# Performance work log

Measured on AMD Instinct MI355X. Metric: run time of the kernel, lower is better.

The kernel has to match this reference:

```python
import jax, jax.numpy as jnp
import numpy as np

PAD_ID, SOS_ID, EOS_ID = 0, 1, 2


def setup_inputs() -> dict:
    key = jax.random.key(0)
    ks = jax.random.split(key, 8)
    V, E, H, B = 16000, 256, 512, 8
    s = 0.05  # weight scale to keep softmax well-conditioned
    return {
        "hidden": jax.random.normal(ks[0], (1, B, H), dtype=jnp.float32),
        "embedding": jax.random.normal(ks[1], (V, E), dtype=jnp.float32) * s,
        "w_ih": jax.random.normal(ks[2], (3 * H, E), dtype=jnp.float32) * s,
        "w_hh": jax.random.normal(ks[3], (3 * H, H), dtype=jnp.float32) * s,
        "b_ih": jax.random.normal(ks[4], (3 * H,), dtype=jnp.float32) * s,
        "b_hh": jax.random.normal(ks[5], (3 * H,), dtype=jnp.float32) * s,
        "w_out": jax.random.normal(ks[6], (V, H), dtype=jnp.float32) * s,
        "b_out": jax.random.normal(ks[7], (V,), dtype=jnp.float32) * s,
        "lenseq": 12,
        "k": 5,
    }


def reference(hidden, embedding, w_ih, w_hh, b_ih, b_hh, w_out, b_out, lenseq, k):
    V, E = embedding.shape
    _, B, H = hidden.shape
    dt = hidden.dtype
    pad_onehot = jax.nn.one_hot(PAD_ID, V, dtype=dt)

    def gru_cell(x_emb, h):  # x_emb: (k,B,E), h: (k,B,H); torch nn.GRU gate order r,z,n
        gi = x_emb @ w_ih.T + b_ih
        gh = h @ w_hh.T + b_hh
        i_r, i_z, i_n = jnp.split(gi, 3, axis=-1)
        h_r, h_z, h_n = jnp.split(gh, 3, axis=-1)
        r = jax.nn.sigmoid(i_r + h_r)
        z = jax.nn.sigmoid(i_z + h_z)
        n = jnp.tanh(i_n + r * h_n)
        return (1.0 - z) * n + z * h

    def step(carry, i):
        x, h, prob, res, _ = carry
        done = (x == EOS_ID) | (x == PAD_ID)            # (k,B)
        emb = embedding[x]                               # (k,B,E)
        h_new = gru_cell(emb, h)                         # (k,B,H)
        probs = jax.nn.softmax(h_new @ w_out.T + b_out, axis=-1)  # (k,B,V)
        pred = jnp.where(done[..., None], pad_onehot, probs)
        h = jnp.where(done[..., None], h, h_new)
        res = res.at[:, i].set(pred)                     # store raw pred (pre prob-scaling), as torch.cat copies
        scores = pred * prob[..., None]                  # (k,B,V); prob stays all-ones, faithful to source
        flat = scores.transpose(1, 0, 2).reshape(B, k * V)  # beam-major flatten per batch elem
        _, idx = jax.lax.top_k(flat, k)                  # (B,k)
        beam = (idx // V).T                              # (k,B)
        tok = (idx % V).T                                # (k,B)
        res = jnp.take_along_axis(res, beam[:, None, :, None], axis=0)
        prob = jnp.take_along_axis(prob, beam, axis=0)
        h = jnp.take_along_axis(h, beam[..., None], axis=0)
        return (tok, h, prob, res, pred), None

    x0 = jnp.full((k, B), SOS_ID, dtype=jnp.int32)
    h0 = jnp.broadcast_to(hidden[0], (k, B, H))
    prob0 = jnp.ones((k, B), dtype=dt)
    res0 = jnp.zeros((k, lenseq, B, V), dtype=dt)
    pred0 = jnp.zeros((k, B, V), dtype=dt)

    (x, h, prob, res, pred), _ = jax.lax.scan(step, (x0, h0, prob0, res0, pred0), jnp.arange(lenseq))

    # final top-1 selection per batch element over (k*V) flat scores
    scores = pred * prob[..., None]
    flat = scores.transpose(1, 0, 2).reshape(B, k * V)
    best_beam = jnp.argmax(flat, axis=-1) // V           # (B,)
    out = jnp.take_along_axis(res, best_beam[None, None, :, None], axis=0)[0]  # (lenseq,B,V)
    return out
```

## Files before the change

### kernel.cpp

```cpp
#include <hip/hip_runtime.h>

#define V 16000
#define E 256
#define H 512
#define HP 516
#define BB 8
#define T 12
#define NB 250
#define NBS 256
#define TPB 1024
#define CPB 64
#define AGENT __HIP_MEMORY_SCOPE_AGENT

typedef float vfloat4 __attribute__((ext_vector_type(4)));


constexpr int W_FL   = CPB * 512;
constexpr int SH_OFF = W_FL;
constexpr int SP_OFF = SH_OFF + BB * HP;
constexpr int RS_OFF = SP_OFF + 64 * 48;
constexpr int RV_OFF = RS_OFF + 128;
constexpr int RI_OFF = RV_OFF + 128;
constexpr int SS_OFF = RI_OFF + 128;
constexpr int XN_OFF = SS_OFF + 8;
constexpr int X_OFF  = XN_OFF + 8;
constexpr int SMEM_FL = X_OFF + 8;
constexpr size_t SMEM_BYTES = (size_t)SMEM_FL * 4;

__device__ __forceinline__ float dot4(float4 a, float4 b) {
    return a.x * b.x + a.y * b.y + a.z * b.z + a.w * b.w;
}

__global__ __launch_bounds__(256) void kinit(const float* __restrict__ hidden,
                                             float* __restrict__ hA,
                                             int* __restrict__ cnt,
                                             int* __restrict__ epoch) {
    int idx = blockIdx.x * 256 + threadIdx.x;
    if (idx < BB * H) hA[idx] = hidden[idx];
    if (idx < 64 * 16) cnt[idx] = 0;
    if (idx == 0) epoch[0] = 0;
}

__device__ __forceinline__ void barA(int* __restrict__ cnt, int ep) {
    __syncthreads();
    if (blockIdx.x < 64 && threadIdx.x == 0)
        __hip_atomic_fetch_add(&cnt[(8 + (blockIdx.x & 1)) * 16], 1,
                               __ATOMIC_RELEASE, AGENT);
    if (threadIdx.x < 2) {
        while (__hip_atomic_load(&cnt[(8 + threadIdx.x) * 16],
                                 __ATOMIC_RELAXED, AGENT) < 32 * ep)
            __builtin_amdgcn_s_sleep(2);
    }
    __builtin_amdgcn_fence(__ATOMIC_ACQUIRE, "workgroup");
    __syncthreads();
}

__device__ __forceinline__ void barB(int* __restrict__ cnt, int ep) {
    __syncthreads();
    if (threadIdx.x == 0)
        __hip_atomic_fetch_add(&cnt[(blockIdx.x & 7) * 16], 1,
                               __ATOMIC_RELEASE, AGENT);
    if (threadIdx.x < 8) {
        int q = (threadIdx.x < 2) ? 32 : 31;
        while (__hip_atomic_load(&cnt[threadIdx.x * 16],
                                 __ATOMIC_RELAXED, AGENT) < q * ep)
            __builtin_amdgcn_s_sleep(2);
    }
    __builtin_amdgcn_fence(__ATOMIC_ACQUIRE, "workgroup");
    __syncthreads();
}

__global__ __launch_bounds__(TPB, 4) void kmain(
    const float* __restrict__ emb_tab,
    const float* __restrict__ w_ih,
    const float* __restrict__ w_hh,
    const float* __restrict__ b_ih,
    const float* __restrict__ b_hh,
    const float* __restrict__ w_out,
    const float* __restrict__ b_out,
    float* __restrict__ hA,
    float* __restrict__ hB,
    float* __restrict__ psum,
    float* __restrict__ pval,
    int* __restrict__ pidx,
    int* __restrict__ cnt,
    int* __restrict__ epoch,
    float* __restrict__ out)
{
    extern __shared__ float smem[];
    float* w_lds  = smem;
    float* s_h    = smem + SH_OFF;
    float* s_part = smem + SP_OFF;
    float* s_e    = smem + SP_OFF;
    float* s_rsum = smem + RS_OFF;
    float* s_rval = smem + RV_OFF;
    int*   s_ridx = (int*)(smem + RI_OFF);
    float* s_S    = smem + SS_OFF;
    int*   s_Xn   = (int*)(smem + XN_OFF);
    int*   s_X    = (int*)(smem + X_OFF);

    const int blk = blockIdx.x, tid = threadIdx.x;
    (void)epoch;

    for (int i = tid; i < CPB * 128; i += TPB) {
        int col = i >> 7;
        int q4  = (i & 127) << 2;
        int vv  = blk * CPB + col;
        float4 w4 = *(const float4*)(w_out + (size_t)vv * H + q4);
        int sw = q4 ^ ((col & 7) << 2) ^ (((q4 >> 5) & 7) << 2);
        *(float4*)(w_lds + col * 512 + sw) = w4;
    }
    if (tid < BB) s_X[tid] = 1;
    __syncthreads();

    const int lane = tid & 63;
    const int wv   = tid >> 6;
    const int rh   = lane & 3;
    const int kq   = (lane >> 2) & 15;
    const int rowhalf = wv & 1;
    const int cs   = wv >> 1;
    const int r    = rowhalf * 4 + rh;
    const int xw   = (cs ^ (kq & 7)) << 2;
    const int hswz = (kq & 7) << 2;

    float bo[8];
#pragma unroll
    for (int p = 0; p < 8; p++) bo[p] = b_out[blk * CPB + p * 8 + cs];

    for (int t = 0; t < T; t++) {
        const float* h_cur = (t & 1) ? hB : hA;
        float*       h_nxt = (t & 1) ? hA : hB;
        const int par = t & 1;

        if (blk < 64) {
            int hr = tid >> 7, k4 = (tid & 127) << 2;
            const unsigned long long* p =
                (const unsigned long long*)(h_cur + hr * H + k4);
            union { unsigned long long u; float f[2]; } c0, c1;
            c0.u = __hip_atomic_load(p,     __ATOMIC_RELAXED, AGENT);
            c1.u = __hip_atomic_load(p + 1, __ATOMIC_RELAXED, AGENT);
            *(float4*)(s_h + hr * HP + k4) =
                make_float4(c0.f[0], c0.f[1], c1.f[0], c1.f[1]);
        }
        __syncthreads();
        if (blk < 64 && tid < 512) {
            const int jl = tid >> 6;
            const int ar = (tid >> 3) & 7;
            const int kq8 = tid & 7;
            const int j  = blk * 8 + jl;
            const int pair = jl * 8 + ar;
            float gir = 0.f, giz = 0.f, gin = 0.f, ghr = 0.f, ghz = 0.f, ghn = 0.f;
            {
                const float* erow = emb_tab + (size_t)s_X[ar] * E;
                const float* w0 = w_ih + (size_t)j * E;
                const float* w1 = w0 + (size_t)H * E;
                const float* w2 = w1 + (size_t)H * E;
                const int k0 = kq8 * (E / 8);
                for (int k = 0; k < E / 8; k += 4) {
                    float4 ev = *(const float4*)(erow + k0 + k);
                    gir += dot4(*(const float4*)(w0 + k0 + k), ev);
                    giz += dot4(*(const float4*)(w1 + k0 + k), ev);
                    gin += dot4(*(const float4*)(w2 + k0 + k), ev);
                }
            }
            {
                const float* hrow = s_h + ar * HP;
                const float* w0 = w_hh + (size_t)j * H;
                const float* w1 = w0 + (size_t)H * H;
                const float* w2 = w1 + (size_t)H * H;
                const int k0 = kq8 * (H / 8);
                for (int k = 0; k < H / 8; k += 4) {
                    float4 hv = *(const float4*)(hrow + k0 + k);
                    ghr += dot4(*(const float4*)(w0 + k0 + k), hv);
                    ghz += dot4(*(const float4*)(w1 + k0 + k), hv);
                    ghn += dot4(*(const float4*)(w2 + k0 + k), hv);
                }
            }
            float* sp = s_part + pair * 48;
            sp[0 * 8 + kq8] = gir; sp[1 * 8 + kq8] = giz; sp[2 * 8 + kq8] = gin;
            sp[3 * 8 + kq8] = ghr; sp[4 * 8 + kq8] = ghz; sp[5 * 8 + kq8] = ghn;
        }
        __syncthreads();
        if (blk < 64 && tid < 512 && (tid & 7) == 0) {
            const int pair = (tid >> 6) * 8 + ((tid >> 3) & 7);
            const int jl = pair >> 3, ar = pair & 7;
            const int j  = blk * 8 + jl;
            const float* sp2 = s_part + pair * 48;
            float G[6];
#pragma unroll
            for (int gg = 0; gg < 6; gg++) {
                float s = 0.f;
#pragma unroll
                for (int q = 0; q < 8; q++) s += sp2[gg * 8 + q];
                G[gg] = s;
            }
            float ir  = G[0] + b_ih[j],         hr_ = G[3] + b_hh[j];
            float iz  = G[1] + b_ih[H + j],     hz  = G[4] + b_hh[H + j];
            float inn = G[2] + b_ih[2 * H + j], hn  = G[5] + b_hh[2 * H + j];
            float rg = 1.f / (1.f + __expf(-(ir + hr_)));
            float zg = 1.f / (1.f + __expf(-(iz + hz)));
            float ng = tanhf(inn + rg * hn);
            float ho = s_h[ar * HP + j];
            int xr = s_X[ar];
            bool dn = (xr == 0) || (xr == 2);
            float hv = dn ? ho : ((1.f - zg) * ng + zg * ho);
            __hip_atomic_store(&h_nxt[ar * H + j], hv, __ATOMIC_RELAXED, AGENT);
        }
        barA(cnt, t + 1);

        {
            int hr = tid >> 7, k4 = (tid & 127) << 2;
            const unsigned long long* p =
                (const unsigned long long*)(h_nxt + hr * H + k4);
            union { unsigned long long u; float f[2]; } c0, c1;
            c0.u = __hip_atomic_load(p,     __ATOMIC_RELAXED, AGENT);
            c1.u = __hip_atomic_load(p + 1, __ATOMIC_RELAXED, AGENT);
            int sw = k4 ^ (((k4 >> 5) & 7) << 2);
            *(float4*)(s_h + hr * HP + sw) =
                make_float4(c0.f[0], c0.f[1], c1.f[0], c1.f[1]);
        }
        __syncthreads();
        {
            float4 hreg[8];
            const float* hb = s_h + r * HP + kq * 32;
#pragma unroll
            for (int i = 0; i < 8; i++)
                hreg[i] = *(const float4*)(hb + ((4 * i) ^ hswz));

            float s_acc = 0.f, bv = -1.f; int bi = 0x7fffffff;
#pragma unroll
            for (int p = 0; p < 8; p++) {
                const int col = p * 8 + cs;
                const int vv  = blk * CPB + col;
                const float* wb = w_lds + col * 512 + kq * 32;
                float acc = 0.f;
#pragma unroll
                for (int i = 0; i < 8; i++) {
                    float4 w4 = *(const float4*)(wb + ((4 * i) ^ xw));
                    acc += dot4(w4, hreg[i]);
                }
                acc += __shfl_xor(acc, 4, 64);
                acc += __shfl_xor(acc, 8, 64);
                acc += __shfl_xor(acc, 16, 64);
                acc += __shfl_xor(acc, 32, 64);
                float ee = __expf(acc + bo[p]);
                if (kq == 0) s_e[r * 65 + col] = ee;
                s_acc += ee;
                if (ee > bv) { bv = ee; bi = vv; }
            }
            if (kq == 0) {
                s_rsum[wv * 8 + r] = s_acc;
                s_rval[wv * 8 + r] = bv;
                s_ridx[wv * 8 + r] = bi;
            } else if (kq == 1) {
                int ro = (1 - rowhalf) * 4 + rh;
                s_rsum[wv * 8 + ro] = 0.f;
                s_rval[wv * 8 + ro] = -1.f;
                s_ridx[wv * 8 + ro] = 0x7fffffff;
            }
        }
        __syncthreads();
        if (tid < 64) {
            float s  = s_rsum[tid] + s_rsum[tid + 64];
            float av = s_rval[tid], bv2 = s_rval[tid + 64];
            int   ai = s_ridx[tid], bi2 = s_ridx[tid + 64];
            float bv = av; int bi = ai;
            if (bv2 > bv || (bv2 == bv && bi2 < bi)) { bv = bv2; bi = bi2; }
#pragma unroll
            for (int m = 8; m <= 32; m <<= 1) {
                s += __shfl_xor(s, m, 64);
                float ov = __shfl_xor(bv, m, 64);
                int   oi = __shfl_xor(bi, m, 64);
                if (ov > bv || (ov == bv && oi < bi)) { bv = ov; bi = oi; }
            }
            if (tid < 8) {
                int o = (par * 8 + tid) * NBS + blk;
                __hip_atomic_store(&psum[o], s,  __ATOMIC_RELAXED, AGENT);
                __hip_atomic_store(&pval[o], bv, __ATOMIC_RELAXED, AGENT);
                __hip_atomic_store(&pidx[o], bi, __ATOMIC_RELAXED, AGENT);
            }
        }
        barB(cnt, t + 1);

        if (wv < 8) {
            const int base = (par * 8 + wv) * NBS;
            float s = 0.f, bv = -1.f; int bi = 0x7fffffff;
#pragma unroll
            for (int c = 0; c < 4; c++) {
                int idx = lane + 64 * c;
                if (idx < NB) {
                    int o = base + idx;
                    s += __hip_atomic_load(&psum[o], __ATOMIC_RELAXED, AGENT);
                    float ov = __hip_atomic_load(&pval[o], __ATOMIC_RELAXED, AGENT);
                    int   oi = __hip_atomic_load(&pidx[o], __ATOMIC_RELAXED, AGENT);
                    if (ov > bv || (ov == bv && oi < bi)) { bv = ov; bi = oi; }
                }
            }
            for (int m = 1; m < 64; m <<= 1) {
                s += __shfl_xor(s, m, 64);
                float ov = __shfl_xor(bv, m, 64);
                int   oi = __shfl_xor(bi, m, 64);
                if (ov > bv || (ov == bv && oi < bi)) { bv = ov; bi = oi; }
            }
            if (lane == 0) { s_S[wv] = s; s_Xn[wv] = bi; }
        }
        __syncthreads();
        {
            float* out_t = out + (size_t)t * BB * V;
            if (tid < 128) {
                int row = tid >> 4;
                int c4  = (tid & 15) << 2;
                int xr = s_X[row];
                bool dn = (xr == 0) || (xr == 2);
                float inv = 1.f / s_S[row];
                int vbase = blk * CPB + c4;
                vfloat4 o4;
                o4.x = dn ? ((vbase + 0 == 0) ? 1.f : 0.f) : s_e[row * 65 + c4 + 0] * inv;
                o4.y = dn ? ((vbase + 1 == 0) ? 1.f : 0.f) : s_e[row * 65 + c4 + 1] * inv;
                o4.z = dn ? ((vbase + 2 == 0) ? 1.f : 0.f) : s_e[row * 65 + c4 + 2] * inv;
                o4.w = dn ? ((vbase + 3 == 0) ? 1.f : 0.f) : s_e[row * 65 + c4 + 3] * inv;
                *(vfloat4*)(out_t + (size_t)row * V + vbase) = o4;
            }
        }
        __syncthreads();
        if (tid < 8) {
            int xo = s_X[tid];
            s_X[tid] = ((xo == 0) || (xo == 2)) ? 0 : s_Xn[tid];
        }
        __syncthreads();
    }
}

extern "C" void kernel_launch(void* const* d_in, const int* in_sizes, int n_in,
                              void* d_out, int out_size, void* d_ws, size_t ws_size,
                              hipStream_t stream) {
    (void)in_sizes; (void)n_in; (void)out_size; (void)ws_size;
    const float* hidden    = (const float*)d_in[0];
    const float* embedding = (const float*)d_in[1];
    const float* w_ih      = (const float*)d_in[2];
    const float* w_hh      = (const float*)d_in[3];
    const float* b_ih      = (const float*)d_in[4];
    const float* b_hh      = (const float*)d_in[5];
    const float* w_out     = (const float*)d_in[6];
    const float* b_out     = (const float*)d_in[7];
    float* out = (float*)d_out;

    float* ws    = (float*)d_ws;
    float* hA    = ws;
    float* hB    = hA + BB * H;
    float* psum  = hB + BB * H;
    float* pval  = psum + 2 * 8 * NBS;
    int*   pidx  = (int*)(pval + 2 * 8 * NBS);
    int*   cnt   = pidx + 2 * 8 * NBS;
    int*   epoch = cnt + 64 * 16;

    hipFuncSetAttribute((const void*)kmain,
        hipFuncAttributeMaxDynamicSharedMemorySize,
        (int)SMEM_BYTES);

    kinit<<<16, 256, 0, stream>>>(hidden, hA, cnt, epoch);
    kmain<<<NB, TPB, SMEM_BYTES, stream>>>(embedding, w_ih, w_hh, b_ih, b_hh,
                                           w_out, b_out, hA, hB, psum, pval,
                                           pidx, cnt, epoch, out);
}
```

Before: 646.2 us.

## Centralize grid barriers and softmax reduction in block zero with broadcast flag

Replaces the all-to-all grid barriers with a gather-then-broadcast scheme. Block 0 alone waits on the per-group counters and reduces the per-block partial sums and argmax candidates. It then publishes the normalizer and next token through a payload area plus a single release flag, and the other blocks spin on that flag instead of each polling eight counters and rereading all partials. The output stores also become nontemporal. This cuts global polling and redundant reduction traffic but serializes the reduction on one block, adding latency on the critical path.

New measurement: 1.240 ms. 91.9% more time.

```diff
diff --git a/kernel.cpp b/kernel.cpp
--- a/kernel.cpp
+++ b/kernel.cpp
@@ -27,6 +27,8 @@
 constexpr int SMEM_FL = X_OFF + 8;
 constexpr size_t SMEM_BYTES = (size_t)SMEM_FL * 4;
 
+constexpr int CNT_LINES = 80;
+
 __device__ __forceinline__ float dot4(float4 a, float4 b) {
     return a.x * b.x + a.y * b.y + a.z * b.z + a.w * b.w;
 }
@@ -37,34 +39,29 @@
                                              int* __restrict__ epoch) {
     int idx = blockIdx.x * 256 + threadIdx.x;
     if (idx < BB * H) hA[idx] = hidden[idx];
-    if (idx < 64 * 16) cnt[idx] = 0;
+    if (idx < CNT_LINES * 16) cnt[idx] = 0;
     if (idx == 0) epoch[0] = 0;
 }
 
 __device__ __forceinline__ void barA(int* __restrict__ cnt, int ep) {
     __syncthreads();
     if (blockIdx.x < 64 && threadIdx.x == 0)
-        __hip_atomic_fetch_add(&cnt[(8 + (blockIdx.x & 1)) * 16], 1,
+        __hip_atomic_fetch_add(&cnt[(64 + (blockIdx.x & 1)) * 16], 1,
                                __ATOMIC_RELEASE, AGENT);
-    if (threadIdx.x < 2) {
-        while (__hip_atomic_load(&cnt[(8 + threadIdx.x) * 16],
-                                 __ATOMIC_RELAXED, AGENT) < 32 * ep)
-            __builtin_amdgcn_s_sleep(2);
-    }
-    __builtin_amdgcn_fence(__ATOMIC_ACQUIRE, "workgroup");
-    __syncthreads();
-}
-
-__device__ __forceinline__ void barB(int* __restrict__ cnt, int ep) {
-    __syncthreads();
-    if (threadIdx.x == 0)
-        __hip_atomic_fetch_add(&cnt[(blockIdx.x & 7) * 16], 1,
-                               __ATOMIC_RELEASE, AGENT);
-    if (threadIdx.x < 8) {
-        int q = (threadIdx.x < 2) ? 32 : 31;
-        while (__hip_atomic_load(&cnt[threadIdx.x * 16],
-                                 __ATOMIC_RELAXED, AGENT) < q * ep)
-            __builtin_amdgcn_s_sleep(2);
+    if (blockIdx.x == 0) {
+        if (threadIdx.x < 2) {
+            while (__hip_atomic_load(&cnt[(64 + threadIdx.x) * 16],
+                                     __ATOMIC_RELAXED, AGENT) < 32 * ep)
+                __builtin_amdgcn_s_sleep(1);
+        }
+        __syncthreads();
+        if (threadIdx.x == 0)
+            __hip_atomic_store(&cnt[63 * 16], ep, __ATOMIC_RELEASE, AGENT);
+    } else {
+        if (threadIdx.x == 0) {
+            while (__hip_atomic_load(&cnt[63 * 16], __ATOMIC_ACQUIRE, AGENT) < ep)
+                __builtin_amdgcn_s_sleep(1);
+        }
     }
     __builtin_amdgcn_fence(__ATOMIC_ACQUIRE, "workgroup");
     __syncthreads();
@@ -100,6 +97,7 @@
     int*   s_X    = (int*)(smem + X_OFF);
 
     const int blk = blockIdx.x, tid = threadIdx.x;
+    int* pay = &cnt[67 * 16];
     (void)epoch;
 
     for (int i = tid; i < CPB * 128; i += TPB) {
@@ -280,31 +278,71 @@
                 __hip_atomic_store(&pidx[o], bi, __ATOMIC_RELAXED, AGENT);
             }
         }
-        barB(cnt, t + 1);
-
-        if (wv < 8) {
-            const int base = (par * 8 + wv) * NBS;
-            float s = 0.f, bv = -1.f; int bi = 0x7fffffff;
-#pragma unroll
-            for (int c = 0; c < 4; c++) {
-                int idx = lane + 64 * c;
-                if (idx < NB) {
-                    int o = base + idx;
-                    s += __hip_atomic_load(&psum[o], __ATOMIC_RELAXED, AGENT);
-                    float ov = __hip_atomic_load(&pval[o], __ATOMIC_RELAXED, AGENT);
-                    int   oi = __hip_atomic_load(&pidx[o], __ATOMIC_RELAXED, AGENT);
+
+        __syncthreads();
+        if (tid == 0) {
+            int g = blk >> 2;
+            __hip_atomic_fetch_add(&cnt[g * 16], 1, __ATOMIC_RELEASE, AGENT);
+        }
+        if (blk == 0) {
+            if (tid < 63) {
+                int expct = (tid == 62) ? 2 : 4;
+                while (__hip_atomic_load(&cnt[tid * 16],
+                                         __ATOMIC_RELAXED, AGENT) < expct * (t + 1))
+                    __builtin_amdgcn_s_sleep(1);
+            }
+            __syncthreads();
+            if (wv < 8) {
+                const int base = (par * 8 + wv) * NBS;
+                float s = 0.f, bv = -1.f; int bi = 0x7fffffff;
+#pragma unroll
+                for (int c = 0; c < 4; c++) {
+                    int idx = lane + 64 * c;
+                    if (idx < NB) {
+                        int o = base + idx;
+                        s += __hip_atomic_load(&psum[o], __ATOMIC_RELAXED, AGENT);
+                        float ov = __hip_atomic_load(&pval[o], __ATOMIC_RELAXED, AGENT);
+                        int   oi = __hip_atomic_load(&pidx[o], __ATOMIC_RELAXED, AGENT);
+                        if (ov > bv || (ov == bv && oi < bi)) { bv = ov; bi = oi; }
+                    }
+                }
+                for (int m = 1; m < 64; m <<= 1) {
+                    s += __shfl_xor(s, m, 64);
+                    float ov = __shfl_xor(bv, m, 64);
+                    int   oi = __shfl_xor(bi, m, 64);
                     if (ov > bv || (ov == bv && oi < bi)) { bv = ov; bi = oi; }
                 }
-            }
-            for (int m = 1; m < 64; m <<= 1) {
-                s += __shfl_xor(s, m, 64);
-                float ov = __shfl_xor(bv, m, 64);
-                int   oi = __shfl_xor(bi, m, 64);
-                if (ov > bv || (ov == bv && oi < bi)) { bv = ov; bi = oi; }
-            }
-            if (lane == 0) { s_S[wv] = s; s_Xn[wv] = bi; }
-        }
-        __syncthreads();
+                if (lane == 0) {
+                    int xo = s_X[wv];
+                    int nx = ((xo == 0) || (xo == 2)) ? 0 : bi;
+                    s_S[wv]  = s;
+                    s_Xn[wv] = nx;
+                    __hip_atomic_store(&pay[wv], __float_as_int(s),
+                                       __ATOMIC_RELAXED, AGENT);
+                    __hip_atomic_store(&pay[8 + wv], nx,
+                                       __ATOMIC_RELAXED, AGENT);
+                }
+            }
+            __syncthreads();
+            if (tid == 0)
+                __hip_atomic_store(&cnt[66 * 16], t + 1, __ATOMIC_RELEASE, AGENT);
+        } else {
+            if (tid == 0) {
+                while (__hip_atomic_load(&cnt[66 * 16],
+                                         __ATOMIC_ACQUIRE, AGENT) < t + 1)
+                    __builtin_amdgcn_s_sleep(1);
+            }
+            __syncthreads();
+            if (tid < 8)
+                s_S[tid] = __int_as_float(
+                    __hip_atomic_load(&pay[tid], __ATOMIC_RELAXED, AGENT));
+            else if (tid < 16)
+                s_Xn[tid - 8] =
+                    __hip_atomic_load(&pay[tid], __ATOMIC_RELAXED, AGENT);
+        }
+        __builtin_amdgcn_fence(__ATOMIC_ACQUIRE, "workgroup");
+        __syncthreads();
+
         {
             float* out_t = out + (size_t)t * BB * V;
             if (tid < 128) {
@@ -319,14 +357,12 @@
                 o4.y = dn ? ((vbase + 1 == 0) ? 1.f : 0.f) : s_e[row * 65 + c4 + 1] * inv;
                 o4.z = dn ? ((vbase + 2 == 0) ? 1.f : 0.f) : s_e[row * 65 + c4 + 2] * inv;
                 o4.w = dn ? ((vbase + 3 == 0) ? 1.f : 0.f) : s_e[row * 65 + c4 + 3] * inv;
-                *(vfloat4*)(out_t + (size_t)row * V + vbase) = o4;
-            }
-        }
-        __syncthreads();
-        if (tid < 8) {
-            int xo = s_X[tid];
-            s_X[tid] = ((xo == 0) || (xo == 2)) ? 0 : s_Xn[tid];
-        }
+                __builtin_nontemporal_store(o4,
+                    (vfloat4*)(out_t + (size_t)row * V + vbase));
+            }
+        }
+        __syncthreads();
+        if (tid < 8) s_X[tid] = s_Xn[tid];
         __syncthreads();
     }
 }
@@ -352,7 +388,7 @@
     float* pval  = psum + 2 * 8 * NBS;
     int*   pidx  = (int*)(pval + 2 * 8 * NBS);
     int*   cnt   = pidx + 2 * 8 * NBS;
-    int*   epoch = cnt + 64 * 16;
+    int*   epoch = cnt + CNT_LINES * 16;
 
     hipFuncSetAttribute((const void*)kmain,
         hipFuncAttributeMaxDynamicSharedMemorySize,
```
